# Optimization experiments

Measured on AMD Instinct MI355X. Metric: run time of the kernel, lower is better.

## Reference

```python
import jax, jax.numpy as jnp
import numpy as np

IN_FEATURES = 1024
OUT_FEATURES = 1024
N_LEAF = 16
BATCH = 4096


def setup_inputs() -> dict:
    key = jax.random.key(0)
    k_x, k_gw, k_pw = jax.random.split(key, 3)
    x = jax.random.normal(k_x, (BATCH, IN_FEATURES), dtype=jnp.float32)
    # xavier_normal for gating weights [in, L]
    gw_std = np.sqrt(2.0 / (IN_FEATURES + N_LEAF))
    gw = jax.random.normal(k_gw, (IN_FEATURES, N_LEAF), dtype=jnp.float32) * gw_std
    gb = jnp.zeros((N_LEAF,), dtype=jnp.float32)
    # kaiming_normal (linear) on [out*L, in] then reshaped to [out, in, L]
    pw_std = np.sqrt(1.0 / IN_FEATURES)
    pw = jax.random.normal(k_pw, (OUT_FEATURES, IN_FEATURES, N_LEAF), dtype=jnp.float32) * pw_std
    pb = jnp.zeros((OUT_FEATURES, N_LEAF), dtype=jnp.float32)
    return {"x": x, "gw": gw, "gb": gb, "pw": pw, "pb": pb}


def reference(x, gw, gb, pw, pb):
    # gatings: softmax over leaves, [B, L]
    g = jax.nn.softmax(x @ gw + gb, axis=1)
    # Fused contraction order (same math as materializing per-sample [out,in]
    # projection matrices): per-leaf projections then gating-weighted sum.
    # leaf_out[b,o,l] = sum_i x[b,i] * pw[o,i,l]
    leaf_out = jnp.einsum('bi,oil->bol', x, pw)
    # result[b,o] = sum_l leaf_out[b,o,l] * g[b,l] + sum_l pb[o,l] * g[b,l]
    result = jnp.einsum('bol,bl->bo', leaf_out, g) + g @ pb.T
    return result
```

## Files before the change

kernel.cpp:

```cpp
#include <hip/hip_runtime.h>
#include <hip/hip_bf16.h>
#include <stdint.h>

#define IN_F   1024
#define OUT_F  1024
#define NLEAF  16
#define BATCH  4096

#define KK      1024
#define NN      (OUT_F * NLEAF)
#define TM      128
#define TN      128
#define BK      32
#define KITERS  (KK / BK)
#define GS_PAD  138

typedef __bf16 bf16x8 __attribute__((ext_vector_type(8)));
typedef float  f32x4  __attribute__((ext_vector_type(4)));

#define ASYNC_COPY16(gp, lp)                                                         \
  __builtin_amdgcn_global_load_lds((const __attribute__((address_space(1))) void*)(gp), \
                                   (__attribute__((address_space(3))) void*)(lp),       \
                                   16, 0, 0)

__global__ __launch_bounds__(256) void prep_kernel(
    const float* __restrict__ x, const float* __restrict__ gw,
    const float* __restrict__ gb, const float* __restrict__ pw,
    float* __restrict__ g, __hip_bfloat16* __restrict__ xb,
    __hip_bfloat16* __restrict__ W) {
  __shared__ __align__(16) __hip_bfloat16 lt[16 * 264];
  const int t = threadIdx.x;

  if (blockIdx.x < OUT_F) {
    const int o = blockIdx.x;
    const float* src = pw + (size_t)o * (IN_F * NLEAF);
    for (int ch = 0; ch < 4; ++ch) {
      const float4* p = (const float4*)(src + ch * 4096 + t * 16);
      const float4 v0 = p[0], v1 = p[1], v2 = p[2], v3 = p[3];
      if (ch) __syncthreads();
      lt[ 0 * 264 + t] = __float2bfloat16(v0.x);
      lt[ 1 * 264 + t] = __float2bfloat16(v0.y);
      lt[ 2 * 264 + t] = __float2bfloat16(v0.z);
      lt[ 3 * 264 + t] = __float2bfloat16(v0.w);
      lt[ 4 * 264 + t] = __float2bfloat16(v1.x);
      lt[ 5 * 264 + t] = __float2bfloat16(v1.y);
      lt[ 6 * 264 + t] = __float2bfloat16(v1.z);
      lt[ 7 * 264 + t] = __float2bfloat16(v1.w);
      lt[ 8 * 264 + t] = __float2bfloat16(v2.x);
      lt[ 9 * 264 + t] = __float2bfloat16(v2.y);
      lt[10 * 264 + t] = __float2bfloat16(v2.z);
      lt[11 * 264 + t] = __float2bfloat16(v2.w);
      lt[12 * 264 + t] = __float2bfloat16(v3.x);
      lt[13 * 264 + t] = __float2bfloat16(v3.y);
      lt[14 * 264 + t] = __float2bfloat16(v3.z);
      lt[15 * 264 + t] = __float2bfloat16(v3.w);
      __syncthreads();
#pragma unroll
      for (int jj = 0; jj < 2; ++jj) {
        const int u = t + 256 * jj;
        const int l = u >> 5;
        const int i8 = (u & 31) * 8;
        *(uint4*)(W + ((size_t)o * NLEAF + l) * KK + ch * 256 + i8) =
            *(const uint4*)(lt + l * 264 + i8);
      }
    }
  } else {
    const int blk  = blockIdx.x - OUT_F;
    const int lane = t & 63;
    const int wv   = t >> 6;
    const int b    = blk * 4 + wv;
    const int i4   = lane >> 4;
    const int l    = lane & 15;

    const float* xrow = x + (size_t)b * IN_F;
    float acc = 0.f;
#pragma unroll 8
    for (int k = 0; k < IN_F / 4; ++k) {
      const float xv = xrow[k * 4 + i4];
      const float wvv = gw[k * 64 + lane];
      acc = fmaf(xv, wvv, acc);
    }
    acc += __shfl_xor(acc, 16);
    acc += __shfl_xor(acc, 32);
    float logit = acc + gb[l];
    float m = logit;
#pragma unroll
    for (int off = 8; off > 0; off >>= 1) m = fmaxf(m, __shfl_xor(m, off));
    float e = __expf(logit - m);
    float s = e;
#pragma unroll
    for (int off = 8; off > 0; off >>= 1) s += __shfl_xor(s, off);
    if (lane < NLEAF) g[b * NLEAF + l] = e / s;

    const float* xblk = x + (size_t)blk * 4 * IN_F;
    __hip_bfloat16* xbblk = xb + (size_t)blk * 4 * IN_F;
#pragma unroll
    for (int j = 0; j < 2; ++j) {
      const int f = (t + 256 * j) * 8;
      const float4 a0 = *(const float4*)(xblk + f);
      const float4 a1 = *(const float4*)(xblk + f + 4);
      __align__(16) __hip_bfloat16 tmp[8];
      tmp[0] = __float2bfloat16(a0.x); tmp[1] = __float2bfloat16(a0.y);
      tmp[2] = __float2bfloat16(a0.z); tmp[3] = __float2bfloat16(a0.w);
      tmp[4] = __float2bfloat16(a1.x); tmp[5] = __float2bfloat16(a1.y);
      tmp[6] = __float2bfloat16(a1.z); tmp[7] = __float2bfloat16(a1.w);
      *(uint4*)(xbblk + f) = *(const uint4*)tmp;
    }
  }
}

__global__ __launch_bounds__(256, 4) void gemm_kernel(
    const __hip_bfloat16* __restrict__ Xb,
    const __hip_bfloat16* __restrict__ W,
    const float* __restrict__ g,
    const float* __restrict__ pb,
    float* __restrict__ out) {
  __shared__ __align__(16) char smem[16384];
  __hip_bfloat16* As = (__hip_bfloat16*)smem;
  __hip_bfloat16* Bs = (__hip_bfloat16*)(smem + 8192);
  float* gs  = (float*)smem;
  float* pbs = (float*)(smem + 8832);

  const int t    = threadIdx.x;
  const int lane = t & 63;
  const int w    = t >> 6;
  const int quad = lane >> 4;
  const int r16  = lane & 15;

  const int b0 = blockIdx.x * TN;
  const int n0 = blockIdx.y * TM;

  const __hip_bfloat16* aG = W + (long)n0 * KK;
  const __hip_bfloat16* bG = Xb + (long)b0 * KK;

  const int  c0 = t, c1 = t + 256;
  const int  sl0 = (c0 & 3) ^ ((c0 >> 3) & 3);
  const int  sl1 = (c1 & 3) ^ ((c1 >> 3) & 3);
  const long aOff0 = (long)(c0 >> 2) * KK + sl0 * 8;
  const long aOff1 = (long)(c1 >> 2) * KK + sl1 * 8;

  const int wn = (w >> 1) * 64;
  const int wb = (w & 1) * 64;
  const int swz = (r16 >> 1) & 3;

  f32x4 acc[4][4] = {};

  for (int it = 0; it < KITERS; ++it) {
    ASYNC_COPY16(aG + aOff0, (char*)As + c0 * 16);
    ASYNC_COPY16(aG + aOff1, (char*)As + c1 * 16);
    ASYNC_COPY16(bG + aOff0, (char*)Bs + c0 * 16);
    ASYNC_COPY16(bG + aOff1, (char*)Bs + c1 * 16);
    __syncthreads();

    bf16x8 af[4], bfr[4];
#pragma unroll
    for (int mi = 0; mi < 4; ++mi)
      af[mi] = *(const bf16x8*)(As + (wn + mi * 16 + r16) * BK + (quad ^ swz) * 8);
#pragma unroll
    for (int ni = 0; ni < 4; ++ni)
      bfr[ni] = *(const bf16x8*)(Bs + (wb + ni * 16 + r16) * BK + (quad ^ swz) * 8);

#pragma unroll
    for (int mi = 0; mi < 4; ++mi)
#pragma unroll
      for (int ni = 0; ni < 4; ++ni)
        acc[mi][ni] = __builtin_amdgcn_mfma_f32_16x16x32_bf16(
            af[mi], bfr[ni], acc[mi][ni], 0, 0, 0);

    __syncthreads();
    aG += BK;
    bG += BK;
  }

#pragma unroll
  for (int j = 0; j < 8; ++j) {
    const int f = t + 256 * j;
    gs[(f & 15) * GS_PAD + (f >> 4)] = g[b0 * NLEAF + f];
  }
  if (t < 128) pbs[t] = pb[n0 + t];
  __syncthreads();

  float pbv[4][4];
#pragma unroll
  for (int mi = 0; mi < 4; ++mi)
#pragma unroll
    for (int r = 0; r < 4; ++r)
      pbv[mi][r] = pbs[((wn >> 4) + mi) * NLEAF + quad * 4 + r];

  const int oBase = (n0 >> 4) + (wn >> 4);
#pragma unroll
  for (int ni = 0; ni < 4; ++ni) {
    const int bl = wb + ni * 16 + r16;
    float gv[4];
#pragma unroll
    for (int r = 0; r < 4; ++r) gv[r] = gs[(quad * 4 + r) * GS_PAD + bl];
    float rv[4];
#pragma unroll
    for (int mi = 0; mi < 4; ++mi) {
      float v = 0.f;
#pragma unroll
      for (int r = 0; r < 4; ++r)
        v = fmaf(acc[mi][ni][r] + pbv[mi][r], gv[r], v);
      v += __shfl_xor(v, 16);
      v += __shfl_xor(v, 32);
      rv[mi] = v;
    }
    if (quad == 0)
      *(float4*)(out + (long)(b0 + bl) * OUT_F + oBase) =
          make_float4(rv[0], rv[1], rv[2], rv[3]);
  }
}

__global__ __launch_bounds__(256) void gate_kernel_fb(
    const float* __restrict__ x, const float* __restrict__ gw,
    const float* __restrict__ gb, float* __restrict__ g) {
  const int lane = threadIdx.x & 63;
  const int wv   = threadIdx.x >> 6;
  const int b    = blockIdx.x * 4 + wv;
  const int i4   = lane >> 4;
  const int l    = lane & 15;
  const float* xrow = x + (size_t)b * IN_F;
  float acc = 0.f;
  for (int k = 0; k < IN_F / 4; ++k)
    acc = fmaf(xrow[k * 4 + i4], gw[k * 64 + lane], acc);
  acc += __shfl_xor(acc, 16);
  acc += __shfl_xor(acc, 32);
  float logit = acc + gb[l];
  float m = logit;
  for (int off = 8; off > 0; off >>= 1) m = fmaxf(m, __shfl_xor(m, off));
  float e = __expf(logit - m);
  float s = e;
  for (int off = 8; off > 0; off >>= 1) s += __shfl_xor(s, off);
  if (lane < NLEAF) g[b * NLEAF + l] = e / s;
}

__global__ __launch_bounds__(256) void fallback_kernel(
    const float* __restrict__ x, const float* __restrict__ pw,
    const float* __restrict__ pb, const float* __restrict__ g,
    float* __restrict__ out) {
  const int b = blockIdx.x;
  __shared__ float xs[IN_F];
  __shared__ float gsl[NLEAF];
  const int t = threadIdx.x;
  for (int j = t; j < IN_F; j += 256) xs[j] = x[(long)b * IN_F + j];
  if (t < NLEAF) gsl[t] = g[b * NLEAF + t];
  __syncthreads();
  for (int o = t; o < OUT_F; o += 256) {
    const float* pwo = pw + (long)o * (IN_F * NLEAF);
    float acc = 0.f;
    for (int i = 0; i < IN_F; ++i) {
      const float xv = xs[i];
      float wsum = 0.f;
#pragma unroll
      for (int l = 0; l < NLEAF; ++l) wsum += gsl[l] * pwo[i * NLEAF + l];
      acc += xv * wsum;
    }
    float bias = 0.f;
#pragma unroll
    for (int l = 0; l < NLEAF; ++l) bias += gsl[l] * pb[o * NLEAF + l];
    out[(long)b * OUT_F + o] = acc + bias;
  }
}

extern "C" void kernel_launch(void* const* d_in, const int* in_sizes, int n_in,
                              void* d_out, int out_size, void* d_ws, size_t ws_size,
                              hipStream_t stream) {
  const float* x  = (const float*)d_in[0];
  const float* gw = (const float*)d_in[1];
  const float* gb = (const float*)d_in[2];
  const float* pw = (const float*)d_in[3];
  const float* pb = (const float*)d_in[4];
  float* out = (float*)d_out;

  const size_t w_bytes  = (size_t)NN * KK * sizeof(__hip_bfloat16);
  const size_t xb_bytes = (size_t)BATCH * KK * sizeof(__hip_bfloat16);
  const size_t g_bytes  = (size_t)BATCH * NLEAF * sizeof(float);

  if (ws_size >= w_bytes + xb_bytes + g_bytes) {
    __hip_bfloat16* W  = (__hip_bfloat16*)d_ws;
    __hip_bfloat16* xb = (__hip_bfloat16*)((char*)d_ws + w_bytes);
    float*          g  = (float*)((char*)d_ws + w_bytes + xb_bytes);

    prep_kernel<<<OUT_F + BATCH / 4, 256, 0, stream>>>(x, gw, gb, pw, g, xb, W);
    gemm_kernel<<<dim3(BATCH / TN, NN / TM), 256, 0, stream>>>(xb, W, g, pb, out);
  } else {
    float* g = (float*)d_ws;
    gate_kernel_fb<<<BATCH / 4, 256, 0, stream>>>(x, gw, gb, g);
    fallback_kernel<<<BATCH, 256, 0, stream>>>(x, pw, pb, g, out);
  }
}
```

Measured before the change: 287.1 us.

## Rewrite GEMM with 256x256 tiles, 4-stage async LDS pipeline and 512 threads

The bf16 GEMM tile grows from 128x128 to 256x256 with 8 waves per block, so each loaded tile is reused across more MFMAs. Global-to-LDS async copies now run through a 4-slot ring buffer with a prefetch depth of 3, explicit vmcnt waits, split barriers and setprio around MFMA bursts, so memory traffic overlaps compute. The epilogue is widened to handle 8 output groups per wave. The cost is 128 KB of dynamic shared memory and more accumulator registers, which lowers occupancy and risks register pressure or spills.

```diff
diff --git a/kernel.cpp b/kernel.cpp
--- a/kernel.cpp
+++ b/kernel.cpp
@@ -9,11 +9,13 @@
 
 #define KK      1024
 #define NN      (OUT_F * NLEAF)
-#define TM      128
-#define TN      128
+#define BM      256
+#define BN      256
 #define BK      32
-#define KITERS  (KK / BK)
-#define GS_PAD  138
+#define NKT     (KK / BK)
+#define ABYTES  (BM * BK * 2)
+#define SLICE   (2 * ABYTES)
+#define GS_PAD  257
 
 typedef __bf16 bf16x8 __attribute__((ext_vector_type(8)));
 typedef float  f32x4  __attribute__((ext_vector_type(4)));
@@ -109,105 +111,166 @@
   }
 }
 
-__global__ __launch_bounds__(256, 4) void gemm_kernel(
+#define STAGE_A(tt)                                                  \
+  do {                                                               \
+    char* _d = smem + (((tt) & 3) * SLICE);                          \
+    const __hip_bfloat16* _s = aG + (long)(tt) * BK;                 \
+    ASYNC_COPY16(_s + gOff0, _d + c0 * 16);                          \
+    ASYNC_COPY16(_s + gOff1, _d + c1 * 16);                          \
+  } while (0)
+
+#define STAGE_B(tt)                                                  \
+  do {                                                               \
+    char* _d = smem + (((tt) & 3) * SLICE) + ABYTES;                 \
+    const __hip_bfloat16* _s = bG + (long)(tt) * BK;                 \
+    ASYNC_COPY16(_s + gOff0, _d + c0 * 16);                          \
+    ASYNC_COPY16(_s + gOff1, _d + c1 * 16);                          \
+  } while (0)
+
+#define TILE_ITER(tt, DO_STAGE, TAILVM)                                        \
+  do {                                                                         \
+    const __hip_bfloat16* As =                                                 \
+        (const __hip_bfloat16*)(smem + ((tt) & 3) * SLICE);                    \
+    const __hip_bfloat16* Bs =                                                 \
+        (const __hip_bfloat16*)(smem + ((tt) & 3) * SLICE + ABYTES);           \
+    bf16x8 af0, af1, af2, af3, bv0, bv1, bv2, bv3;                             \
+    af0 = *(const bf16x8*)(As + ((wr * 128 +  0 + r16) * 4 + (quad ^ swz)) * 8); \
+    af1 = *(const bf16x8*)(As + ((wr * 128 + 16 + r16) * 4 + (quad ^ swz)) * 8); \
+    af2 = *(const bf16x8*)(As + ((wr * 128 + 32 + r16) * 4 + (quad ^ swz)) * 8); \
+    af3 = *(const bf16x8*)(As + ((wr * 128 + 48 + r16) * 4 + (quad ^ swz)) * 8); \
+    bv0 = *(const bf16x8*)(Bs + ((wc * 64 +  0 + r16) * 4 + (quad ^ swz)) * 8);  \
+    bv1 = *(const bf16x8*)(Bs + ((wc * 64 + 16 + r16) * 4 + (quad ^ swz)) * 8);  \
+    bv2 = *(const bf16x8*)(Bs + ((wc * 64 + 32 + r16) * 4 + (quad ^ swz)) * 8);  \
+    bv3 = *(const bf16x8*)(Bs + ((wc * 64 + 48 + r16) * 4 + (quad ^ swz)) * 8);  \
+    if (DO_STAGE) STAGE_A((tt) + 3);                                           \
+    __builtin_amdgcn_s_barrier();                                              \
+    asm volatile("s_waitcnt lgkmcnt(0)" ::: "memory");                         \
+    __builtin_amdgcn_sched_barrier(0);                                         \
+    __builtin_amdgcn_s_setprio(1);                                             \
+    acc[0][0] = __builtin_amdgcn_mfma_f32_16x16x32_bf16(af0, bv0, acc[0][0], 0, 0, 0); \
+    acc[0][1] = __builtin_amdgcn_mfma_f32_16x16x32_bf16(af0, bv1, acc[0][1], 0, 0, 0); \
+    acc[0][2] = __builtin_amdgcn_mfma_f32_16x16x32_bf16(af0, bv2, acc[0][2], 0, 0, 0); \
+    acc[0][3] = __builtin_amdgcn_mfma_f32_16x16x32_bf16(af0, bv3, acc[0][3], 0, 0, 0); \
+    acc[1][0] = __builtin_amdgcn_mfma_f32_16x16x32_bf16(af1, bv0, acc[1][0], 0, 0, 0); \
+    acc[1][1] = __builtin_amdgcn_mfma_f32_16x16x32_bf16(af1, bv1, acc[1][1], 0, 0, 0); \
+    acc[1][2] = __builtin_amdgcn_mfma_f32_16x16x32_bf16(af1, bv2, acc[1][2], 0, 0, 0); \
+    acc[1][3] = __builtin_amdgcn_mfma_f32_16x16x32_bf16(af1, bv3, acc[1][3], 0, 0, 0); \
+    acc[2][0] = __builtin_amdgcn_mfma_f32_16x16x32_bf16(af2, bv0, acc[2][0], 0, 0, 0); \
+    acc[2][1] = __builtin_amdgcn_mfma_f32_16x16x32_bf16(af2, bv1, acc[2][1], 0, 0, 0); \
+    acc[2][2] = __builtin_amdgcn_mfma_f32_16x16x32_bf16(af2, bv2, acc[2][2], 0, 0, 0); \
+    acc[2][3] = __builtin_amdgcn_mfma_f32_16x16x32_bf16(af2, bv3, acc[2][3], 0, 0, 0); \
+    acc[3][0] = __builtin_amdgcn_mfma_f32_16x16x32_bf16(af3, bv0, acc[3][0], 0, 0, 0); \
+    acc[3][1] = __builtin_amdgcn_mfma_f32_16x16x32_bf16(af3, bv1, acc[3][1], 0, 0, 0); \
+    acc[3][2] = __builtin_amdgcn_mfma_f32_16x16x32_bf16(af3, bv2, acc[3][2], 0, 0, 0); \
+    acc[3][3] = __builtin_amdgcn_mfma_f32_16x16x32_bf16(af3, bv3, acc[3][3], 0, 0, 0); \
+    __builtin_amdgcn_s_setprio(0);                                             \
+    __builtin_amdgcn_s_barrier();                                              \
+    af0 = *(const bf16x8*)(As + ((wr * 128 +  64 + r16) * 4 + (quad ^ swz)) * 8); \
+    af1 = *(const bf16x8*)(As + ((wr * 128 +  80 + r16) * 4 + (quad ^ swz)) * 8); \
+    af2 = *(const bf16x8*)(As + ((wr * 128 +  96 + r16) * 4 + (quad ^ swz)) * 8); \
+    af3 = *(const bf16x8*)(As + ((wr * 128 + 112 + r16) * 4 + (quad ^ swz)) * 8); \
+    if (DO_STAGE) STAGE_B((tt) + 3);                                           \
+    TAILVM;                                                                    \
+    __builtin_amdgcn_s_barrier();                                              \
+    asm volatile("s_waitcnt lgkmcnt(0)" ::: "memory");                         \
+    __builtin_amdgcn_sched_barrier(0);                                         \
+    __builtin_amdgcn_s_setprio(1);                                             \
+    acc[4][0] = __builtin_amdgcn_mfma_f32_16x16x32_bf16(af0, bv0, acc[4][0], 0, 0, 0); \
+    acc[4][1] = __builtin_amdgcn_mfma_f32_16x16x32_bf16(af0, bv1, acc[4][1], 0, 0, 0); \
+    acc[4][2] = __builtin_amdgcn_mfma_f32_16x16x32_bf16(af0, bv2, acc[4][2], 0, 0, 0); \
+    acc[4][3] = __builtin_amdgcn_mfma_f32_16x16x32_bf16(af0, bv3, acc[4][3], 0, 0, 0); \
+    acc[5][0] = __builtin_amdgcn_mfma_f32_16x16x32_bf16(af1, bv0, acc[5][0], 0, 0, 0); \
+    acc[5][1] = __builtin_amdgcn_mfma_f32_16x16x32_bf16(af1, bv1, acc[5][1], 0, 0, 0); \
+    acc[5][2] = __builtin_amdgcn_mfma_f32_16x16x32_bf16(af1, bv2, acc[5][2], 0, 0, 0); \
+    acc[5][3] = __builtin_amdgcn_mfma_f32_16x16x32_bf16(af1, bv3, acc[5][3], 0, 0, 0); \
+    acc[6][0] = __builtin_amdgcn_mfma_f32_16x16x32_bf16(af2, bv0, acc[6][0], 0, 0, 0); \
+    acc[6][1] = __builtin_amdgcn_mfma_f32_16x16x32_bf16(af2, bv1, acc[6][1], 0, 0, 0); \
+    acc[6][2] = __builtin_amdgcn_mfma_f32_16x16x32_bf16(af2, bv2, acc[6][2], 0, 0, 0); \
+    acc[6][3] = __builtin_amdgcn_mfma_f32_16x16x32_bf16(af2, bv3, acc[6][3], 0, 0, 0); \
+    acc[7][0] = __builtin_amdgcn_mfma_f32_16x16x32_bf16(af3, bv0, acc[7][0], 0, 0, 0); \
+    acc[7][1] = __builtin_amdgcn_mfma_f32_16x16x32_bf16(af3, bv1, acc[7][1], 0, 0, 0); \
+    acc[7][2] = __builtin_amdgcn_mfma_f32_16x16x32_bf16(af3, bv2, acc[7][2], 0, 0, 0); \
+    acc[7][3] = __builtin_amdgcn_mfma_f32_16x16x32_bf16(af3, bv3, acc[7][3], 0, 0, 0); \
+    __builtin_amdgcn_s_setprio(0);                                             \
+    __builtin_amdgcn_s_barrier();                                              \
+  } while (0)
+
+__global__ __launch_bounds__(512, 2) void gemm_kernel(
     const __hip_bfloat16* __restrict__ Xb,
     const __hip_bfloat16* __restrict__ W,
     const float* __restrict__ g,
     const float* __restrict__ pb,
     float* __restrict__ out) {
-  __shared__ __align__(16) char smem[16384];
-  __hip_bfloat16* As = (__hip_bfloat16*)smem;
-  __hip_bfloat16* Bs = (__hip_bfloat16*)(smem + 8192);
-  float* gs  = (float*)smem;
-  float* pbs = (float*)(smem + 8832);
+  extern __shared__ __align__(16) char smem[];
 
   const int t    = threadIdx.x;
   const int lane = t & 63;
   const int w    = t >> 6;
   const int quad = lane >> 4;
   const int r16  = lane & 15;
-
-  const int b0 = blockIdx.x * TN;
-  const int n0 = blockIdx.y * TM;
-
-  const __hip_bfloat16* aG = W + (long)n0 * KK;
+  const int wr   = w >> 2;
+  const int wc   = w & 3;
+  const int swz  = (r16 >> 1) & 3;
+
+  const int b0 = blockIdx.x * BN;
+  const int n0 = blockIdx.y * BM;
+
+  const __hip_bfloat16* aG = W  + (long)n0 * KK;
   const __hip_bfloat16* bG = Xb + (long)b0 * KK;
 
-  const int  c0 = t, c1 = t + 256;
-  const int  sl0 = (c0 & 3) ^ ((c0 >> 3) & 3);
-  const int  sl1 = (c1 & 3) ^ ((c1 >> 3) & 3);
-  const long aOff0 = (long)(c0 >> 2) * KK + sl0 * 8;
-  const long aOff1 = (long)(c1 >> 2) * KK + sl1 * 8;
-
-  const int wn = (w >> 1) * 64;
-  const int wb = (w & 1) * 64;
-  const int swz = (r16 >> 1) & 3;
-
-  f32x4 acc[4][4] = {};
-
-  for (int it = 0; it < KITERS; ++it) {
-    ASYNC_COPY16(aG + aOff0, (char*)As + c0 * 16);
-    ASYNC_COPY16(aG + aOff1, (char*)As + c1 * 16);
-    ASYNC_COPY16(bG + aOff0, (char*)Bs + c0 * 16);
-    ASYNC_COPY16(bG + aOff1, (char*)Bs + c1 * 16);
-    __syncthreads();
-
-    bf16x8 af[4], bfr[4];
-#pragma unroll
-    for (int mi = 0; mi < 4; ++mi)
-      af[mi] = *(const bf16x8*)(As + (wn + mi * 16 + r16) * BK + (quad ^ swz) * 8);
-#pragma unroll
-    for (int ni = 0; ni < 4; ++ni)
-      bfr[ni] = *(const bf16x8*)(Bs + (wb + ni * 16 + r16) * BK + (quad ^ swz) * 8);
-
-#pragma unroll
-    for (int mi = 0; mi < 4; ++mi)
-#pragma unroll
-      for (int ni = 0; ni < 4; ++ni)
-        acc[mi][ni] = __builtin_amdgcn_mfma_f32_16x16x32_bf16(
-            af[mi], bfr[ni], acc[mi][ni], 0, 0, 0);
-
-    __syncthreads();
-    aG += BK;
-    bG += BK;
-  }
-
+  const int  c0 = t, c1 = t + 512;
+  const long gOff0 = (long)(c0 >> 2) * KK + (long)(((c0 & 3) ^ ((c0 >> 3) & 3)) * 8);
+  const long gOff1 = (long)(c1 >> 2) * KK + (long)(((c1 & 3) ^ ((c1 >> 3) & 3)) * 8);
+
+  f32x4 acc[8][4] = {};
+
+  STAGE_A(0); STAGE_B(0);
+  STAGE_A(1); STAGE_B(1);
+  STAGE_A(2); STAGE_B(2);
+  asm volatile("s_waitcnt vmcnt(8)" ::: "memory");
+  __builtin_amdgcn_s_barrier();
+
+  for (int tt = 0; tt < NKT - 3; ++tt)
+    TILE_ITER(tt, 1, asm volatile("s_waitcnt vmcnt(8)" ::: "memory"));
+  TILE_ITER(NKT - 3, 0, asm volatile("s_waitcnt vmcnt(4)" ::: "memory"));
+  TILE_ITER(NKT - 2, 0, asm volatile("s_waitcnt vmcnt(0)" ::: "memory"));
+  TILE_ITER(NKT - 1, 0, (void)0);
+
+  float* gs  = (float*)smem;
+  float* pbs = (float*)(smem + 16 * GS_PAD * 4);
 #pragma unroll
   for (int j = 0; j < 8; ++j) {
-    const int f = t + 256 * j;
+    const int f = t + 512 * j;
     gs[(f & 15) * GS_PAD + (f >> 4)] = g[b0 * NLEAF + f];
   }
-  if (t < 128) pbs[t] = pb[n0 + t];
+  if (t < 256) pbs[t] = pb[(n0 >> 4) * NLEAF + t];
   __syncthreads();
 
-  float pbv[4][4];
-#pragma unroll
-  for (int mi = 0; mi < 4; ++mi)
-#pragma unroll
-    for (int r = 0; r < 4; ++r)
-      pbv[mi][r] = pbs[((wn >> 4) + mi) * NLEAF + quad * 4 + r];
-
-  const int oBase = (n0 >> 4) + (wn >> 4);
+  const int oBase = (n0 >> 4) + wr * 8;
 #pragma unroll
   for (int ni = 0; ni < 4; ++ni) {
-    const int bl = wb + ni * 16 + r16;
+    const int bl = wc * 64 + ni * 16 + r16;
     float gv[4];
 #pragma unroll
     for (int r = 0; r < 4; ++r) gv[r] = gs[(quad * 4 + r) * GS_PAD + bl];
-    float rv[4];
-#pragma unroll
-    for (int mi = 0; mi < 4; ++mi) {
+    float rv[8];
+#pragma unroll
+    for (int mi = 0; mi < 8; ++mi) {
       float v = 0.f;
 #pragma unroll
       for (int r = 0; r < 4; ++r)
-        v = fmaf(acc[mi][ni][r] + pbv[mi][r], gv[r], v);
+        v = fmaf(acc[mi][ni][r] + pbs[(wr * 8 + mi) * NLEAF + quad * 4 + r],
+                 gv[r], v);
       v += __shfl_xor(v, 16);
       v += __shfl_xor(v, 32);
       rv[mi] = v;
     }
-    if (quad == 0)
+    if (quad == 0) {
       *(float4*)(out + (long)(b0 + bl) * OUT_F + oBase) =
           make_float4(rv[0], rv[1], rv[2], rv[3]);
+      *(float4*)(out + (long)(b0 + bl) * OUT_F + oBase + 4) =
+          make_float4(rv[4], rv[5], rv[6], rv[7]);
+    }
   }
 }
 
@@ -281,8 +344,17 @@
     __hip_bfloat16* xb = (__hip_bfloat16*)((char*)d_ws + w_bytes);
     float*          g  = (float*)((char*)d_ws + w_bytes + xb_bytes);
 
+    static int attr_done = 0;
+    if (!attr_done) {
+      (void)hipFuncSetAttribute((const void*)gemm_kernel,
+                                hipFuncAttributeMaxDynamicSharedMemorySize,
+                                4 * SLICE);
+      attr_done = 1;
+    }
+
     prep_kernel<<<OUT_F + BATCH / 4, 256, 0, stream>>>(x, gw, gb, pw, g, xb, W);
-    gemm_kernel<<<dim3(BATCH / TN, NN / TM), 256, 0, stream>>>(xb, W, g, pb, out);
+    gemm_kernel<<<dim3(BATCH / BN, NN / BM), 512, 4 * SLICE, stream>>>(
+        xb, W, g, pb, out);
   } else {
     float* g = (float*)d_ws;
     gate_kernel_fb<<<BATCH / 4, 256, 0, stream>>>(x, gw, gb, g);
```

Result: faster. 259.4 us (-9.6%).

## Rewrite GEMM with 256x256 tiles, 4-stage async LDS pipeline and 32x32 MFMA

Applied to the files above, without the earlier changes.

Replaces the 128x128 single-buffered GEMM tile with a 256x256 tile that uses 128KB of dynamic LDS as a 4-deep ring of async global-to-LDS copies. Fine-grained vmcnt waits and a single barrier per k-tile replace the two syncthreads per iteration. Fragment register double-buffering overlaps LDS reads with 32x32x16 MFMAs. The gating epilogue is re-mapped to the 32x32 accumulator layout. The larger tile raises arithmetic intensity and hides memory latency, at the cost of one block per CU and 256 registers of accumulators per thread, which risks spills.

```diff
diff --git a/kernel.cpp b/kernel.cpp
--- a/kernel.cpp
+++ b/kernel.cpp
@@ -9,19 +9,24 @@
 
 #define KK      1024
 #define NN      (OUT_F * NLEAF)
-#define TM      128
-#define TN      128
+#define BM      256
+#define BN      256
 #define BK      32
-#define KITERS  (KK / BK)
-#define GS_PAD  138
+#define NKT     (KK / BK)
+#define BUFB    32768
+#define GS_PAD  257
 
 typedef __bf16 bf16x8 __attribute__((ext_vector_type(8)));
-typedef float  f32x4  __attribute__((ext_vector_type(4)));
+typedef float  f32x16 __attribute__((ext_vector_type(16)));
 
 #define ASYNC_COPY16(gp, lp)                                                         \
   __builtin_amdgcn_global_load_lds((const __attribute__((address_space(1))) void*)(gp), \
                                    (__attribute__((address_space(3))) void*)(lp),       \
                                    16, 0, 0)
+
+#define VM8  asm volatile("s_waitcnt vmcnt(8)" ::: "memory")
+#define VM0  asm volatile("s_waitcnt vmcnt(0)" ::: "memory")
+#define NOVM ((void)0)
 
 __global__ __launch_bounds__(256) void prep_kernel(
     const float* __restrict__ x, const float* __restrict__ gw,
@@ -109,105 +114,158 @@
   }
 }
 
-__global__ __launch_bounds__(256, 4) void gemm_kernel(
+#define STAGE(ktt)                                                             \
+  do {                                                                         \
+    char* _b = smem + ((ktt) & 3) * BUFB;                                      \
+    const __hip_bfloat16* _sa = aG + (long)(ktt) * BK;                         \
+    const __hip_bfloat16* _sb = bG + (long)(ktt) * BK;                         \
+    ASYNC_COPY16(_sa + gO,                _b + t * 16);                        \
+    ASYNC_COPY16(_sa + gO +  64 * KK,     _b + t * 16 + 4096);                 \
+    ASYNC_COPY16(_sa + gO + 128 * KK,     _b + t * 16 + 8192);                 \
+    ASYNC_COPY16(_sa + gO + 192 * KK,     _b + t * 16 + 12288);                \
+    ASYNC_COPY16(_sb + gO,                _b + 16384 + t * 16);                \
+    ASYNC_COPY16(_sb + gO +  64 * KK,     _b + 16384 + t * 16 + 4096);         \
+    ASYNC_COPY16(_sb + gO + 128 * KK,     _b + 16384 + t * 16 + 8192);         \
+    ASYNC_COPY16(_sb + gO + 192 * KK,     _b + 16384 + t * 16 + 12288);        \
+  } while (0)
+
+#define RDA(D0, D1, D2, D3, U, KX)                                             \
+  do {                                                                         \
+    const char* _p = smem + (U) * BUFB + aRow + (KX);                          \
+    D0 = *(const bf16x8*)(_p);                                                 \
+    D1 = *(const bf16x8*)(_p + 2048);                                          \
+    D2 = *(const bf16x8*)(_p + 4096);                                          \
+    D3 = *(const bf16x8*)(_p + 6144);                                          \
+  } while (0)
+
+#define RDB(D0, D1, D2, D3, U, KX)                                             \
+  do {                                                                         \
+    const char* _p = smem + (U) * BUFB + bRow + (KX);                          \
+    D0 = *(const bf16x8*)(_p);                                                 \
+    D1 = *(const bf16x8*)(_p + 2048);                                          \
+    D2 = *(const bf16x8*)(_p + 4096);                                          \
+    D3 = *(const bf16x8*)(_p + 6144);                                          \
+  } while (0)
+
+#define MFMA16(A0, A1, A2, A3, B0, B1, B2, B3)                                 \
+  acc[0][0] = __builtin_amdgcn_mfma_f32_32x32x16_bf16(A0, B0, acc[0][0], 0, 0, 0); \
+  acc[0][1] = __builtin_amdgcn_mfma_f32_32x32x16_bf16(A0, B1, acc[0][1], 0, 0, 0); \
+  acc[0][2] = __builtin_amdgcn_mfma_f32_32x32x16_bf16(A0, B2, acc[0][2], 0, 0, 0); \
+  acc[0][3] = __builtin_amdgcn_mfma_f32_32x32x16_bf16(A0, B3, acc[0][3], 0, 0, 0); \
+  acc[1][0] = __builtin_amdgcn_mfma_f32_32x32x16_bf16(A1, B0, acc[1][0], 0, 0, 0); \
+  acc[1][1] = __builtin_amdgcn_mfma_f32_32x32x16_bf16(A1, B1, acc[1][1], 0, 0, 0); \
+  acc[1][2] = __builtin_amdgcn_mfma_f32_32x32x16_bf16(A1, B2, acc[1][2], 0, 0, 0); \
+  acc[1][3] = __builtin_amdgcn_mfma_f32_32x32x16_bf16(A1, B3, acc[1][3], 0, 0, 0); \
+  acc[2][0] = __builtin_amdgcn_mfma_f32_32x32x16_bf16(A2, B0, acc[2][0], 0, 0, 0); \
+  acc[2][1] = __builtin_amdgcn_mfma_f32_32x32x16_bf16(A2, B1, acc[2][1], 0, 0, 0); \
+  acc[2][2] = __builtin_amdgcn_mfma_f32_32x32x16_bf16(A2, B2, acc[2][2], 0, 0, 0); \
+  acc[2][3] = __builtin_amdgcn_mfma_f32_32x32x16_bf16(A2, B3, acc[2][3], 0, 0, 0); \
+  acc[3][0] = __builtin_amdgcn_mfma_f32_32x32x16_bf16(A3, B0, acc[3][0], 0, 0, 0); \
+  acc[3][1] = __builtin_amdgcn_mfma_f32_32x32x16_bf16(A3, B1, acc[3][1], 0, 0, 0); \
+  acc[3][2] = __builtin_amdgcn_mfma_f32_32x32x16_bf16(A3, B2, acc[3][2], 0, 0, 0); \
+  acc[3][3] = __builtin_amdgcn_mfma_f32_32x32x16_bf16(A3, B3, acc[3][3], 0, 0, 0);
+
+#define KTILE(kt, DOSTAGE, DOPRE, TAILVM, DOBAR)                               \
+  do {                                                                         \
+    if (DOSTAGE) STAGE((kt) + 3);                                              \
+    RDA(p0, p1, p2, p3, (kt) & 3, kx1);                                        \
+    RDB(q0, q1, q2, q3, (kt) & 3, kx1);                                        \
+    MFMA16(a0, a1, a2, a3, b0, b1, b2, b3);                                    \
+    if (DOPRE) {                                                               \
+      RDA(a0, a1, a2, a3, ((kt) + 1) & 3, kx0);                                \
+      RDB(b0, b1, b2, b3, ((kt) + 1) & 3, kx0);                                \
+    }                                                                          \
+    MFMA16(p0, p1, p2, p3, q0, q1, q2, q3);                                    \
+    TAILVM;                                                                    \
+    if (DOBAR) __builtin_amdgcn_s_barrier();                                   \
+  } while (0)
+
+__global__ __launch_bounds__(256, 1) void gemm_kernel(
     const __hip_bfloat16* __restrict__ Xb,
     const __hip_bfloat16* __restrict__ W,
     const float* __restrict__ g,
     const float* __restrict__ pb,
     float* __restrict__ out) {
-  __shared__ __align__(16) char smem[16384];
-  __hip_bfloat16* As = (__hip_bfloat16*)smem;
-  __hip_bfloat16* Bs = (__hip_bfloat16*)(smem + 8192);
-  float* gs  = (float*)smem;
-  float* pbs = (float*)(smem + 8832);
+  extern __shared__ __align__(16) char smem[];
 
   const int t    = threadIdx.x;
   const int lane = t & 63;
   const int w    = t >> 6;
-  const int quad = lane >> 4;
-  const int r16  = lane & 15;
-
-  const int b0 = blockIdx.x * TN;
-  const int n0 = blockIdx.y * TM;
-
-  const __hip_bfloat16* aG = W + (long)n0 * KK;
-  const __hip_bfloat16* bG = Xb + (long)b0 * KK;
-
-  const int  c0 = t, c1 = t + 256;
-  const int  sl0 = (c0 & 3) ^ ((c0 >> 3) & 3);
-  const int  sl1 = (c1 & 3) ^ ((c1 >> 3) & 3);
-  const long aOff0 = (long)(c0 >> 2) * KK + sl0 * 8;
-  const long aOff1 = (long)(c1 >> 2) * KK + sl1 * 8;
-
-  const int wn = (w >> 1) * 64;
-  const int wb = (w & 1) * 64;
-  const int swz = (r16 >> 1) & 3;
-
-  f32x4 acc[4][4] = {};
-
-  for (int it = 0; it < KITERS; ++it) {
-    ASYNC_COPY16(aG + aOff0, (char*)As + c0 * 16);
-    ASYNC_COPY16(aG + aOff1, (char*)As + c1 * 16);
-    ASYNC_COPY16(bG + aOff0, (char*)Bs + c0 * 16);
-    ASYNC_COPY16(bG + aOff1, (char*)Bs + c1 * 16);
-    __syncthreads();
-
-    bf16x8 af[4], bfr[4];
-#pragma unroll
-    for (int mi = 0; mi < 4; ++mi)
-      af[mi] = *(const bf16x8*)(As + (wn + mi * 16 + r16) * BK + (quad ^ swz) * 8);
-#pragma unroll
-    for (int ni = 0; ni < 4; ++ni)
-      bfr[ni] = *(const bf16x8*)(Bs + (wb + ni * 16 + r16) * BK + (quad ^ swz) * 8);
-
-#pragma unroll
-    for (int mi = 0; mi < 4; ++mi)
-#pragma unroll
-      for (int ni = 0; ni < 4; ++ni)
-        acc[mi][ni] = __builtin_amdgcn_mfma_f32_16x16x32_bf16(
-            af[mi], bfr[ni], acc[mi][ni], 0, 0, 0);
-
-    __syncthreads();
-    aG += BK;
-    bG += BK;
-  }
-
-#pragma unroll
-  for (int j = 0; j < 8; ++j) {
+  const int r32  = lane & 31;
+  const int h    = lane >> 5;
+  const int wr   = w >> 1;
+  const int wc   = w & 1;
+
+  const int b0_ = blockIdx.x * BN;
+  const int n0  = blockIdx.y * BM;
+
+  const __hip_bfloat16* aG = W  + (long)n0 * KK;
+  const __hip_bfloat16* bG = Xb + (long)b0_ * KK;
+
+  const long gO = (long)(t >> 2) * KK + (long)(((t & 3) ^ ((t >> 3) & 3)) * 8);
+
+  const int sw  = (r32 >> 1) & 3;
+  const int kx0 = ((0 + h) ^ sw) * 16;
+  const int kx1 = ((2 + h) ^ sw) * 16;
+  const int aRow = (wr * 128 + r32) * 64;
+  const int bRow = 16384 + (wc * 128 + r32) * 64;
+
+  f32x16 acc[4][4] = {};
+  bf16x8 a0, a1, a2, a3, b0, b1, b2, b3;
+  bf16x8 p0, p1, p2, p3, q0, q1, q2, q3;
+
+  STAGE(0); STAGE(1); STAGE(2);
+  VM8;
+  __builtin_amdgcn_s_barrier();
+  RDA(a0, a1, a2, a3, 0, kx0);
+  RDB(b0, b1, b2, b3, 0, kx0);
+
+  for (int kt = 0; kt < NKT - 4; kt += 4) {
+    KTILE(kt + 0, 1, 1, VM8, 1);
+    KTILE(kt + 1, 1, 1, VM8, 1);
+    KTILE(kt + 2, 1, 1, VM8, 1);
+    KTILE(kt + 3, 1, 1, VM8, 1);
+  }
+  KTILE(NKT - 4, 1, 1, VM8, 1);
+  KTILE(NKT - 3, 0, 1, VM0, 1);
+  KTILE(NKT - 2, 0, 1, NOVM, 0);
+  KTILE(NKT - 1, 0, 0, NOVM, 0);
+
+  __syncthreads();
+  float* gs  = (float*)smem;
+  float* pbs = (float*)(smem + 16 * GS_PAD * 4);
+#pragma unroll
+  for (int j = 0; j < 16; ++j) {
     const int f = t + 256 * j;
-    gs[(f & 15) * GS_PAD + (f >> 4)] = g[b0 * NLEAF + f];
-  }
-  if (t < 128) pbs[t] = pb[n0 + t];
+    gs[(f & 15) * GS_PAD + (f >> 4)] = g[b0_ * NLEAF + f];
+  }
+  pbs[t] = pb[(n0 >> 4) * NLEAF + t];
   __syncthreads();
 
-  float pbv[4][4];
-#pragma unroll
-  for (int mi = 0; mi < 4; ++mi)
-#pragma unroll
-    for (int r = 0; r < 4; ++r)
-      pbv[mi][r] = pbs[((wn >> 4) + mi) * NLEAF + quad * 4 + r];
-
-  const int oBase = (n0 >> 4) + (wn >> 4);
-#pragma unroll
-  for (int ni = 0; ni < 4; ++ni) {
-    const int bl = wb + ni * 16 + r16;
-    float gv[4];
-#pragma unroll
-    for (int r = 0; r < 4; ++r) gv[r] = gs[(quad * 4 + r) * GS_PAD + bl];
-    float rv[4];
-#pragma unroll
-    for (int mi = 0; mi < 4; ++mi) {
-      float v = 0.f;
-#pragma unroll
-      for (int r = 0; r < 4; ++r)
-        v = fmaf(acc[mi][ni][r] + pbv[mi][r], gv[r], v);
-      v += __shfl_xor(v, 16);
-      v += __shfl_xor(v, 32);
-      rv[mi] = v;
-    }
-    if (quad == 0)
-      *(float4*)(out + (long)(b0 + bl) * OUT_F + oBase) =
-          make_float4(rv[0], rv[1], rv[2], rv[3]);
+  const int oBase = (n0 >> 4) + wr * 8;
+#pragma unroll
+  for (int bj = 0; bj < 4; ++bj) {
+    const int bl = wc * 128 + bj * 32 + r32;
+    float gv[8];
+#pragma unroll
+    for (int j = 0; j < 8; ++j)
+      gv[j] = gs[((j & 3) + 8 * ((j >> 2) & 1) + 4 * h) * GS_PAD + bl];
+#pragma unroll
+    for (int bi = 0; bi < 4; ++bi) {
+      const int o0 = wr * 8 + bi * 2;
+      float v0 = 0.f, v1 = 0.f;
+#pragma unroll
+      for (int j = 0; j < 8; ++j) {
+        const int l = (j & 3) + 8 * ((j >> 2) & 1) + 4 * h;
+        v0 = fmaf(acc[bi][bj][j]     + pbs[o0 * NLEAF + l],       gv[j], v0);
+        v1 = fmaf(acc[bi][bj][j + 8] + pbs[(o0 + 1) * NLEAF + l], gv[j], v1);
+      }
+      v0 += __shfl_xor(v0, 32);
+      v1 += __shfl_xor(v1, 32);
+      if (h == 0)
+        *(float2*)(out + (long)(b0_ + bl) * OUT_F + oBase + bi * 2) =
+            make_float2(v0, v1);
+    }
   }
 }
 
@@ -281,8 +339,17 @@
     __hip_bfloat16* xb = (__hip_bfloat16*)((char*)d_ws + w_bytes);
     float*          g  = (float*)((char*)d_ws + w_bytes + xb_bytes);
 
+    static int attr_done = 0;
+    if (!attr_done) {
+      (void)hipFuncSetAttribute((const void*)gemm_kernel,
+                                hipFuncAttributeMaxDynamicSharedMemorySize,
+                                131072);
+      attr_done = 1;
+    }
+
     prep_kernel<<<OUT_F + BATCH / 4, 256, 0, stream>>>(x, gw, gb, pw, g, xb, W);
-    gemm_kernel<<<dim3(BATCH / TN, NN / TM), 256, 0, stream>>>(xb, W, g, pb, out);
+    gemm_kernel<<<dim3(BATCH / BN, NN / BM), 256, 131072, stream>>>(
+        xb, W, g, pb, out);
   } else {
     float* g = (float*)d_ws;
     gate_kernel_fb<<<BATCH / 4, 256, 0, stream>>>(x, gw, gb, g);
```

New measurement: 281.2 us. 2.1% less time.
